# Kernel optimization log

Measured on AMD Instinct MI355X. Metric: run time of the kernel, lower is better.

## Reference

```python
import jax, jax.numpy as jnp
import numpy as np

N_NODES = 50000
N_EDGES = 800000
N_INPUT = 512
N_HIDDEN = 64


def setup_inputs() -> dict:
    key = jax.random.key(0)
    ks = jax.random.split(key, 6)
    x = jax.random.normal(ks[0], (1, N_NODES, N_INPUT), dtype=jnp.float32)
    edge_rows = jax.random.randint(ks[1], (N_EDGES,), 0, N_NODES, dtype=jnp.int64)
    edge_cols = jax.random.randint(ks[2], (N_EDGES,), 0, N_NODES, dtype=jnp.int64)
    edge_vals = jax.random.uniform(ks[3], (N_EDGES,), dtype=jnp.float32)
    # xavier_normal_ on fc.weight: std = sqrt(2 / (fan_in + fan_out))
    std = float(np.sqrt(2.0 / (N_INPUT + N_HIDDEN)))
    W = jax.random.normal(ks[4], (N_HIDDEN, N_INPUT), dtype=jnp.float32) * std
    b = jnp.zeros((N_HIDDEN,), dtype=jnp.float32)
    alpha = jnp.full((1,), 0.25, dtype=jnp.float32)  # PReLU default init
    return {"x": x, "edge_rows": edge_rows, "edge_cols": edge_cols,
            "edge_vals": edge_vals, "W": W, "b": b, "alpha": alpha}


def reference(x, edge_rows, edge_cols, edge_vals, W, b, alpha):
    # Linear projection: [1, N, F_in] @ [F_in, F_out] -> [1, N, F_out]
    h = jnp.einsum('bnf,hf->bnh', x, W) + b
    h = jnp.squeeze(h, 0)  # [N, F_out]
    # spmm(adj, h): out[i] = sum_e vals[e] * h[cols[e]] for rows[e] == i
    msgs = edge_vals[:, None] * h[edge_cols]  # [E, F_out]
    agg = jax.ops.segment_sum(msgs, edge_rows, num_segments=N_NODES)  # [N, F_out]
    out = agg[None, :, :]  # [1, N, F_out]
    # PReLU with shared alpha
    return jnp.where(out >= 0, out, alpha * out)
```

## Files before the change

### kernel.cpp

```cpp
#include <hip/hip_runtime.h>

#define NODES 50000
#define NEDGES 800000
#define NIN 512
#define NHID 64
#define CAP 64

typedef __attribute__((ext_vector_type(8))) short short8v;
typedef __attribute__((ext_vector_type(8))) unsigned short ushort8v;
typedef __attribute__((ext_vector_type(4))) float f32x4;

#define H_OFF    0
#define WBF_OFF  1600000
#define CNT_OFF  1616384
#define ECV_OFF  1666384

__device__ inline unsigned short f2bf(float f) {
  unsigned u = __builtin_bit_cast(unsigned, f);
  u += 0x7FFF + ((u >> 16) & 1);
  return (unsigned short)(u >> 16);
}
__device__ inline float bf2f(unsigned short u) {
  return __builtin_bit_cast(float, (unsigned)u << 16);
}

__global__ __launch_bounds__(256) void init_kernel(
    const float* __restrict__ W, unsigned int* __restrict__ wbf,
    int* __restrict__ cnt)
{
  int i = blockIdx.x * 256 + threadIdx.x;
  if (i < NIN * NHID / 2) {
    float2 w = reinterpret_cast<const float2*>(W)[i];
    wbf[i] = (unsigned)f2bf(w.x) | ((unsigned)f2bf(w.y) << 16);
  }
  if (i < NODES) cnt[i] = 0;
}

__global__ __launch_bounds__(64) void fat_kernel(
    const float* __restrict__ x, const unsigned short* __restrict__ wbf,
    const float* __restrict__ b, unsigned short* __restrict__ h,
    const int* __restrict__ rows, const int* __restrict__ cols,
    const float* __restrict__ vals, int* __restrict__ cnt,
    int2* __restrict__ ecv)
{
  int bid = blockIdx.x;

  if (bid & 1) {
    int t = (bid >> 1) * 64 + (int)threadIdx.x;
    int e0 = t * 4;
    int4   r4 = *reinterpret_cast<const int4*>(rows + e0);
    int4   c4 = *reinterpret_cast<const int4*>(cols + e0);
    float4 v4 = *reinterpret_cast<const float4*>(vals + e0);
    int s0 = atomicAdd(&cnt[r4.x], 1);
    int s1 = atomicAdd(&cnt[r4.y], 1);
    int s2 = atomicAdd(&cnt[r4.z], 1);
    int s3 = atomicAdd(&cnt[r4.w], 1);
    if (s0 < CAP) ecv[(long)r4.x * CAP + s0] = make_int2(c4.x, __float_as_int(v4.x));
    if (s1 < CAP) ecv[(long)r4.y * CAP + s1] = make_int2(c4.y, __float_as_int(v4.y));
    if (s2 < CAP) ecv[(long)r4.z * CAP + s2] = make_int2(c4.z, __float_as_int(v4.z));
    if (s3 < CAP) ecv[(long)r4.w * CAP + s3] = make_int2(c4.w, __float_as_int(v4.w));
    return;
  }

  int gw = bid >> 1;
  int lane = (int)(threadIdx.x & 63);
  int r16 = lane & 15;
  int kg  = lane >> 4;

  const float4* xp = reinterpret_cast<const float4*>(
      x + (long)(gw * 16 + r16) * NIN + kg * 8);
  const unsigned short* wp = wbf + (long)r16 * NIN + kg * 8;

  float4 xb[32];
  #pragma unroll
  for (int s = 0; s < 16; ++s) {
    xb[2 * s]     = xp[8 * s];
    xb[2 * s + 1] = xp[8 * s + 1];
  }

  f32x4 acc[4] = {{0,0,0,0},{0,0,0,0},{0,0,0,0},{0,0,0,0}};

  #pragma unroll
  for (int s = 0; s < 16; ++s) {
    float4 a0 = xb[2 * s];
    float4 a1 = xb[2 * s + 1];
    short8v af;
    af[0] = (short)f2bf(a0.x); af[1] = (short)f2bf(a0.y);
    af[2] = (short)f2bf(a0.z); af[3] = (short)f2bf(a0.w);
    af[4] = (short)f2bf(a1.x); af[5] = (short)f2bf(a1.y);
    af[6] = (short)f2bf(a1.z); af[7] = (short)f2bf(a1.w);
    #pragma unroll
    for (int ft = 0; ft < 4; ++ft) {
      short8v bfr = *reinterpret_cast<const short8v*>(
          wp + (long)ft * 16 * NIN + s * 32);
      acc[ft] = __builtin_amdgcn_mfma_f32_16x16x32_bf16(af, bfr, acc[ft], 0, 0, 0);
    }
  }

  int n0 = gw * 16 + kg * 4;
  #pragma unroll
  for (int ft = 0; ft < 4; ++ft) {
    float bias = b[ft * 16 + r16];
    #pragma unroll
    for (int r = 0; r < 4; ++r)
      h[(long)(n0 + r) * NHID + ft * 16 + r16] = f2bf(acc[ft][r] + bias);
  }
}

__global__ __launch_bounds__(256) void gather_kernel(
    const int* __restrict__ cnt, const int2* __restrict__ ecv,
    const unsigned short* __restrict__ h, const float* __restrict__ alpha,
    float* __restrict__ out)
{
  int wid = (int)((blockIdx.x * 256 + threadIdx.x) >> 6);
  if (wid >= NODES) return;
  int lane = (int)(threadIdx.x & 63);
  int eg = lane >> 3;
  int fo = lane & 7;
  int deg = cnt[wid];
  if (deg > CAP) deg = CAP;
  const int2* base = ecv + (long)wid * CAP;
  float a = alpha[0];

  float acc[8] = {0.f, 0.f, 0.f, 0.f, 0.f, 0.f, 0.f, 0.f};
  int j = eg;
  int2 e = (j < deg) ? base[j] : make_int2(0, 0);
  while (j < deg) {
    int2 en = (j + 8 < deg) ? base[j + 8] : make_int2(0, 0);
    float v = __int_as_float(e.y);
    ushort8v hv = *reinterpret_cast<const ushort8v*>(&h[(long)e.x * NHID + fo * 8]);
    #pragma unroll
    for (int k = 0; k < 8; ++k)
      acc[k] = fmaf(v, bf2f(hv[k]), acc[k]);
    e = en;
    j += 8;
  }

  #pragma unroll
  for (int k = 0; k < 8; ++k) {
    acc[k] += __shfl_xor(acc[k], 8);
    acc[k] += __shfl_xor(acc[k], 16);
    acc[k] += __shfl_xor(acc[k], 32);
  }

  if (eg == 0) {
    float4 o0, o1;
    o0.x = acc[0] >= 0.f ? acc[0] : a * acc[0];
    o0.y = acc[1] >= 0.f ? acc[1] : a * acc[1];
    o0.z = acc[2] >= 0.f ? acc[2] : a * acc[2];
    o0.w = acc[3] >= 0.f ? acc[3] : a * acc[3];
    o1.x = acc[4] >= 0.f ? acc[4] : a * acc[4];
    o1.y = acc[5] >= 0.f ? acc[5] : a * acc[5];
    o1.z = acc[6] >= 0.f ? acc[6] : a * acc[6];
    o1.w = acc[7] >= 0.f ? acc[7] : a * acc[7];
    *reinterpret_cast<float4*>(&out[(long)wid * NHID + fo * 8]) = o0;
    *reinterpret_cast<float4*>(&out[(long)wid * NHID + fo * 8 + 4]) = o1;
  }
}

extern "C" void kernel_launch(void* const* d_in, const int* in_sizes, int n_in,
                              void* d_out, int out_size, void* d_ws, size_t ws_size,
                              hipStream_t stream) {
  const float* x     = (const float*)d_in[0];
  const int*   rows  = (const int*)d_in[1];
  const int*   cols  = (const int*)d_in[2];
  const float* vals  = (const float*)d_in[3];
  const float* W     = (const float*)d_in[4];
  const float* b     = (const float*)d_in[5];
  const float* alpha = (const float*)d_in[6];
  float* out = (float*)d_out;

  float* wsf = (float*)d_ws;
  unsigned short* h   = (unsigned short*)(wsf + H_OFF);
  unsigned int*   wbf = (unsigned int*)(wsf + WBF_OFF);
  int*            cnt = (int*)(wsf + CNT_OFF);
  int2*           ecv = (int2*)(wsf + ECV_OFF);

  init_kernel<<<(NODES + 255) / 256, 256, 0, stream>>>(W, wbf, cnt);
  fat_kernel<<<6250, 64, 0, stream>>>(
      x, (const unsigned short*)wbf, b, h, rows, cols, vals, cnt, ecv);
  gather_kernel<<<NODES * 64 / 256, 256, 0, stream>>>(cnt, ecv, h, alpha, out);
}
```

Baseline: 103.9 us.

## Partition edge scatter by row range so each block group writes a localized slice

The edge-bucketing blocks now each own one of 8 row ranges and scan all edges, inserting only those whose row falls in their range. Scatter writes and atomics on cnt/ecv then land in a narrower address region per block group, which may improve L2/XCD locality. The cost is that the rows/cols/vals arrays are read 8 times, and the GEMM blocks now come after all scatter blocks instead of being interleaved with them.

```diff
diff --git a/kernel.cpp b/kernel.cpp
--- a/kernel.cpp
+++ b/kernel.cpp
@@ -5,6 +5,9 @@
 #define NIN 512
 #define NHID 64
 #define CAP 64
+#define NQUAD 200000
+#define BB 2048
+#define ROWS_PER_G (NODES / 8)
 
 typedef __attribute__((ext_vector_type(8))) short short8v;
 typedef __attribute__((ext_vector_type(8))) unsigned short ushort8v;
@@ -45,24 +48,38 @@
 {
   int bid = blockIdx.x;
 
-  if (bid & 1) {
-    int t = (bid >> 1) * 64 + (int)threadIdx.x;
-    int e0 = t * 4;
-    int4   r4 = *reinterpret_cast<const int4*>(rows + e0);
-    int4   c4 = *reinterpret_cast<const int4*>(cols + e0);
-    float4 v4 = *reinterpret_cast<const float4*>(vals + e0);
-    int s0 = atomicAdd(&cnt[r4.x], 1);
-    int s1 = atomicAdd(&cnt[r4.y], 1);
-    int s2 = atomicAdd(&cnt[r4.z], 1);
-    int s3 = atomicAdd(&cnt[r4.w], 1);
-    if (s0 < CAP) ecv[(long)r4.x * CAP + s0] = make_int2(c4.x, __float_as_int(v4.x));
-    if (s1 < CAP) ecv[(long)r4.y * CAP + s1] = make_int2(c4.y, __float_as_int(v4.y));
-    if (s2 < CAP) ecv[(long)r4.z * CAP + s2] = make_int2(c4.z, __float_as_int(v4.z));
-    if (s3 < CAP) ecv[(long)r4.w * CAP + s3] = make_int2(c4.w, __float_as_int(v4.w));
+  if (bid < BB) {
+    int g = bid & 7;
+    int sub = bid >> 3;
+    int r_lo = g * ROWS_PER_G;
+    int r_hi = r_lo + ROWS_PER_G;
+
+    for (int q = sub * 64 + (int)threadIdx.x; q < NQUAD; q += (BB / 8) * 64) {
+      int e0 = q * 4;
+      int4   r4 = *reinterpret_cast<const int4*>(rows + e0);
+      int4   c4 = *reinterpret_cast<const int4*>(cols + e0);
+      float4 v4 = *reinterpret_cast<const float4*>(vals + e0);
+      if (r4.x >= r_lo && r4.x < r_hi) {
+        int s = atomicAdd(&cnt[r4.x], 1);
+        if (s < CAP) ecv[(long)r4.x * CAP + s] = make_int2(c4.x, __float_as_int(v4.x));
+      }
+      if (r4.y >= r_lo && r4.y < r_hi) {
+        int s = atomicAdd(&cnt[r4.y], 1);
+        if (s < CAP) ecv[(long)r4.y * CAP + s] = make_int2(c4.y, __float_as_int(v4.y));
+      }
+      if (r4.z >= r_lo && r4.z < r_hi) {
+        int s = atomicAdd(&cnt[r4.z], 1);
+        if (s < CAP) ecv[(long)r4.z * CAP + s] = make_int2(c4.z, __float_as_int(v4.z));
+      }
+      if (r4.w >= r_lo && r4.w < r_hi) {
+        int s = atomicAdd(&cnt[r4.w], 1);
+        if (s < CAP) ecv[(long)r4.w * CAP + s] = make_int2(c4.w, __float_as_int(v4.w));
+      }
+    }
     return;
   }
 
-  int gw = bid >> 1;
+  int gw = bid - BB;
   int lane = (int)(threadIdx.x & 63);
   int r16 = lane & 15;
   int kg  = lane >> 4;
@@ -177,7 +194,7 @@
   int2*           ecv = (int2*)(wsf + ECV_OFF);
 
   init_kernel<<<(NODES + 255) / 256, 256, 0, stream>>>(W, wbf, cnt);
-  fat_kernel<<<6250, 64, 0, stream>>>(
+  fat_kernel<<<BB + NODES / 16, 64, 0, stream>>>(
       x, (const unsigned short*)wbf, b, h, rows, cols, vals, cnt, ecv);
   gather_kernel<<<NODES * 64 / 256, 256, 0, stream>>>(cnt, ecv, h, alpha, out);
 }
```

After: 89.60 us. -13.8%, faster.
